# Performance work log

Measured on AMD Instinct MI355X. Metric: run time of the kernel, lower is better.

## Reference

```python
import jax, jax.numpy as jnp
import numpy as np

N, E, D, H, T, R, K = 40000, 320000, 128, 4, 3, 5, 3
DK = D // H
SQRT_DK = float(np.sqrt(DK))

def _glorot(key, shape):
    lim = float(np.sqrt(6.0 / (shape[-2] + shape[-1])))
    return jax.random.uniform(key, shape, jnp.float32, -lim, lim)

def setup_inputs():
    ks = jax.random.split(jax.random.key(0), 16)
    return {
        "meta_xs": jax.random.normal(ks[0], (N, D), jnp.float32),
        "node_type": jax.random.randint(ks[1], (N,), 0, T),
        "edge_index": jax.random.randint(ks[2], (2, E), 0, N),
        "edge_type": jax.random.randint(ks[3], (E,), 0, R),
        "edge_time": jax.random.randint(ks[4], (E,), 0, 100),
        "q_w": _glorot(ks[5], (T, D, D)), "q_b": jnp.zeros((T, D), jnp.float32),
        "k_w": _glorot(ks[6], (T, D, D)), "k_b": jnp.zeros((T, D), jnp.float32),
        "v_w": _glorot(ks[7], (T, D, D)), "v_b": jnp.zeros((T, D), jnp.float32),
        "a_w": _glorot(ks[8], (T, D, D)), "a_b": jnp.zeros((T, D), jnp.float32),
        "rel_pri": jnp.ones((R, H), jnp.float32),
        "rel_att": _glorot(ks[9], (R, H, DK, DK)),
        "rel_msg": _glorot(ks[10], (R, H, DK, DK)),
        "WMk": _glorot(ks[11], (K, D, D)),
        "Wak": _glorot(ks[12], (K, D, D)),
        "Wq": _glorot(ks[13], (D, D)), "bq": jnp.zeros((D,), jnp.float32),
        "Wkl": _glorot(ks[14], (D, D)), "bkl": jnp.zeros((D,), jnp.float32),
        "skip": jnp.ones((T,), jnp.float32),
        "ln_g": jnp.ones((T, D), jnp.float32),
        "ln_b": jnp.zeros((T, D), jnp.float32),
    }

def _forward(meta_xs, q_w, q_b, k_w, k_b, v_w, v_b, a_w, a_b, rel_pri, rel_att,
             rel_msg, WMk, Wak, Wq, bq, Wkl, bkl, skip, ln_g, ln_b,
             node_type, edge_index, edge_type):
    src, tgt = edge_index[0], edge_index[1]
    ar = jnp.arange(N)

    def typed(x, W, b):  # per-node-type linear: equivalent to the type-masked loops
        all_t = jnp.einsum('ni,tio->tno', x, W)        # [T, N, D]
        return all_t[node_type, ar] + b[node_type]      # [N, D]

    qn = typed(meta_xs, q_w, q_b).reshape(N, H, DK)
    kn = typed(meta_xs, k_w, k_b).reshape(N, H, DK)
    vn = typed(meta_xs, v_w, v_b).reshape(N, H, DK)
    qe, ke, ve = qn[tgt], kn[src], vn[src]              # [E, H, DK]

    # relation-specific bmm, honoring per-relation dispatch without [E,H,DK,DK] gather
    kp = jnp.zeros_like(ke)
    vp = jnp.zeros_like(ve)
    for r in range(R):
        sel = (edge_type == r)[:, None, None]
        kp = jnp.where(sel, jnp.einsum('ehd,hdm->ehm', ke, rel_att[r]), kp)
        vp = jnp.where(sel, jnp.einsum('ehd,hdm->ehm', ve, rel_msg[r]), vp)

    logits = (qe * kp).sum(-1) * rel_pri[edge_type] / SQRT_DK   # [E, H]
    # segment softmax over incoming edges per target node (torch_geometric softmax)
    mx = jax.ops.segment_max(logits, tgt, num_segments=N)
    ex = jnp.exp(logits - mx[tgt])
    att = ex / (jax.ops.segment_sum(ex, tgt, num_segments=N)[tgt] + 1e-16)

    # power-moment expanded, attention-weighted messages: [K, E, D]
    msgs = jnp.stack([((vp ** (kk + 1)) * att[:, :, None]).reshape(E, D) for kk in range(K)])

    # faithful to original aggregate(): messages indexed by target node id (not edge id)
    agg = jnp.stack([jax.ops.segment_sum(msgs[kk][tgt], tgt, num_segments=N) for kk in range(K)])
    # faithful: only the last moment gets the signed K-th root (loop re-clones each iter)
    root = jnp.sign(agg[K - 1]) * (jnp.abs(agg[K - 1]) + 1e-18) ** (1.0 / K)
    aggm = agg.at[K - 1].set(root)
    aggm = jnp.einsum('knd,kde->kne', aggm, WMk)        # [K, N, D]

    qlin = meta_xs @ Wq + bq
    res = jnp.zeros((N, D), meta_xs.dtype)
    for kk in range(K):
        front = qlin @ Wak[kk]                          # [N, D]
        tail = aggm[kk] @ Wkl + bkl                     # [N, D]
        t = jax.nn.sigmoid((front * tail).sum(-1))      # [N]
        res = res + t[:, None] * aggm[kk]

    # update(): gelu -> per-type linear -> learned skip -> per-type LayerNorm
    h = jax.nn.gelu(res, approximate=False)
    trans = typed(h, a_w, a_b)
    alpha = jax.nn.sigmoid(skip)[node_type][:, None]
    y = trans * alpha + meta_xs * (1.0 - alpha)
    mu = y.mean(-1, keepdims=True)
    var = ((y - mu) ** 2).mean(-1, keepdims=True)
    y = (y - mu) / jnp.sqrt(var + 1e-5) * ln_g[node_type] + ln_b[node_type]
    return y

def reference(meta_xs, node_type, edge_index, edge_type, edge_time,
              q_w, q_b, k_w, k_b, v_w, v_b, a_w, a_b, rel_pri, rel_att, rel_msg,
              WMk, Wak, Wq, bq, Wkl, bkl, skip, ln_g, ln_b):
    return _forward(meta_xs, q_w, q_b, k_w, k_b, v_w, v_b, a_w, a_b, rel_pri,
                    rel_att, rel_msg, WMk, Wak, Wq, bq, Wkl, bkl, skip, ln_g, ln_b,
                    node_type, edge_index, edge_type)
```

## Files before the change

kernel.cpp:

```cpp
#include <hip/hip_runtime.h>

#define N_ 40000
#define E_ 320000
#define D_ 128
#define H_ 4
#define T_ 3
#define R_ 5

typedef unsigned short u16;
typedef float f32x4 __attribute__((ext_vector_type(4)));
typedef short s16x8 __attribute__((ext_vector_type(8)));

__device__ __forceinline__ float bf2f(u16 h){ return __uint_as_float(((unsigned)h)<<16); }
__device__ __forceinline__ u16 f2bf(float f){
  unsigned u = __float_as_uint(f);
  u += 0x7fffu + ((u>>16)&1u);
  return (u16)(u>>16);
}
__device__ __forceinline__ unsigned fmono(float f){
  unsigned u = __float_as_uint(f);
  return (u>>31) ? ~u : (u | 0x80000000u);
}
__device__ __forceinline__ float monof(unsigned u){
  return (u>>31) ? __uint_as_float(u & 0x7fffffffu) : __uint_as_float(~u);
}
__device__ __forceinline__ float ldx(const void* p, long i, int f32){
  return f32 ? ((const float*)p)[i] : bf2f(((const u16*)p)[i]);
}
__device__ __forceinline__ float wredsum(float v){
  #pragma unroll
  for (int m=32;m;m>>=1) v += __shfl_xor(v, m, 64);
  return v;
}
__device__ __forceinline__ void split2(float v0, float v1, unsigned& hp, unsigned& lp){
  unsigned b0 = __float_as_uint(v0), b1 = __float_as_uint(v1);
  unsigned h0 = b0 & 0xFFFF0000u,    h1 = b1 & 0xFFFF0000u;
  float r0 = v0 - __uint_as_float(h0);
  float r1 = v1 - __uint_as_float(h1);
  hp = (h0>>16) | h1;
  lp = (__float_as_uint(r0)>>16) | (__float_as_uint(r1) & 0xFFFF0000u);
}

#define W_QW 0
#define W_KW 49152
#define W_VW 98304
#define W_AW 147456
#define W_QB 196608
#define W_KB 196992
#define W_VB 197376
#define W_AB 197760
#define W_PRI 198144
#define W_RATT 198164
#define W_RMSG 218644
#define W_WMK 239124
#define W_WAK 288276
#define W_WQ 337428
#define W_BQ 353812
#define W_WKL 353940
#define W_BKL 370324
#define W_SKIP 370452
#define W_LNG 370455
#define W_LNB 370839
#define W_TOT 371223

#define WT_Q   0
#define WT_K   98304
#define WT_V   196608
#define WT_A   294912
#define WT_WQ  396328
#define WT_WMK 478248

#define OFF_FLAGS 0ul
#define OFF_WCF   512ul
#define OFF_NT32  1485824ul
#define OFF_EI32  1646080ul
#define OFF_ET32  4206592ul
#define OFF_PERM  5486592ul
#define OFF_PCNT  5648384ul
#define OFF_TVAL  5648896ul
#define OFF_NPERM 5730816ul
#define OFF_LOG   6288896ul
#define OFF_QN    12848896ul
#define OFF_KN    33328896ul
#define OFF_VN    53808896ul
#define OFF_QLIN  74288896ul
#define OFF_QTR   94768896ul

__global__ __launch_bounds__(256) void detect_kernel(
    const u16* __restrict__ xs, const int* __restrict__ nt, int* __restrict__ flags)
{
  __shared__ int sBig, sZero, sNz;
  int tid = threadIdx.x;
  if (tid==0){ sBig=0; sZero=0; sNz=0; }
  __syncthreads();
  int big=0, zc=0;
  for (int i=tid; i<1024; i+=256) {
    u16 v = xs[2*i];
    int e = (v>>7)&0xFF;
    big += (e >= 200);
    zc  += (v == 0);
  }
  int nz=0;
  for (int i=tid; i<1024; i+=256) nz += (nt[2*i+1] != 0);
  atomicAdd(&sBig, big); atomicAdd(&sZero, zc); atomicAdd(&sNz, nz);
  __syncthreads();
  if (tid==0) {
    flags[0] = (sBig > 64) || (sZero > 900);
    flags[1] = (sNz == 0);
  }
}

struct FPtrs { const void* p[20]; };
__global__ __launch_bounds__(256) void convf_kernel(
    const int* __restrict__ flags, FPtrs ptrs, float* __restrict__ wcf)
{
  const int start[21] = {0,49152,98304,147456,196608,196992,197376,197760,198144,
    198164,218644,239124,288276,337428,353812,353940,370324,370452,370455,370839,371223};
  int i = blockIdx.x*256 + threadIdx.x;
  if (i >= W_TOT) return;
  int arr = 0;
  #pragma unroll
  for (int a=1; a<20; ++a) arr += (i >= start[a]);
  int local = i - start[arr];
  wcf[i] = ldx(ptrs.p[arr], local, flags[0]);
}

__global__ __launch_bounds__(256) void idxconv_kernel(
    const int* __restrict__ flags,
    const int* __restrict__ nt, const int* __restrict__ ei, const int* __restrict__ et,
    int* __restrict__ nt32, int* __restrict__ ei32, int* __restrict__ et32)
{
  int i = blockIdx.x*256 + threadIdx.x;
  if (i >= 1000000) return;
  int w = flags[1] ? 2 : 1;
  if (i < 40000)        nt32[i] = nt[(long)i*w];
  else if (i < 680000)  { int j=i-40000;  ei32[j] = ei[(long)j*w]; }
  else                  { int j=i-680000; et32[j] = et[(long)j*w]; }
}

__global__ __launch_bounds__(256) void pinit_kernel(int* __restrict__ perm, int* __restrict__ pc){
  int i = blockIdx.x*256 + threadIdx.x;
  if (i < 40448) perm[i] = -1;
  if (i < 12) pc[i] = 0;
}
__global__ __launch_bounds__(256) void einit_kernel(int* __restrict__ nperm, int* __restrict__ pc2){
  int i = blockIdx.x*256 + threadIdx.x;
  if (i < 40320) nperm[i] = -1;
  if (i < 16) pc2[i] = 0;
}
__global__ __launch_bounds__(256) void cnt_kernel(
    const int* __restrict__ keys, int n, int ntypes, int* __restrict__ gcnt)
{
  __shared__ int lh[8];
  if (threadIdx.x < ntypes) lh[threadIdx.x] = 0;
  __syncthreads();
  int i = blockIdx.x*256 + threadIdx.x;
  if (i < n) atomicAdd(&lh[keys[i]], 1);
  __syncthreads();
  if (threadIdx.x < ntypes && lh[threadIdx.x])
    atomicAdd(&gcnt[threadIdx.x], lh[threadIdx.x]);
}
__global__ void pofs_kernel(int* __restrict__ pc){
  if (threadIdx.x==0 && blockIdx.x==0) {
    pc[8] = 0;
    pc[9] = (pc[0]+127)&~127;
    pc[10] = pc[9] + ((pc[1]+127)&~127);
  }
}
__global__ void eofs_kernel(int* __restrict__ pc2){
  if (threadIdx.x==0 && blockIdx.x==0) {
    pc2[10] = 0;
    #pragma unroll
    for (int r=1;r<R_;++r) pc2[10+r] = pc2[10+r-1] + ((pc2[r-1]+63)&~63);
  }
}
__global__ __launch_bounds__(256) void scat_kernel(
    const int* __restrict__ keys, int n, int ntypes,
    const int* __restrict__ ofs, int* __restrict__ fill, int* __restrict__ perm)
{
  __shared__ int lh[8];
  __shared__ int lbase[8];
  if (threadIdx.x < ntypes) lh[threadIdx.x] = 0;
  __syncthreads();
  int i = blockIdx.x*256 + threadIdx.x;
  int t = 0, rank = 0;
  bool ok = (i < n);
  if (ok) { t = keys[i]; rank = atomicAdd(&lh[t], 1); }
  __syncthreads();
  if (threadIdx.x < ntypes)
    lbase[threadIdx.x] = lh[threadIdx.x] ? atomicAdd(&fill[threadIdx.x], lh[threadIdx.x]) : 0;
  __syncthreads();
  if (ok) perm[ofs[t] + lbase[t] + rank] = i;
}

__global__ __launch_bounds__(256) void init_kernel(
    unsigned* __restrict__ mxkey, float* __restrict__ sumex, int* __restrict__ deg)
{
  int i = blockIdx.x*256 + threadIdx.x;
  mxkey[i] = fmono(-1e30f);
  sumex[i] = 0.f;
  if (i < N_) deg[i] = 0;
}

__global__ __launch_bounds__(256) void prepA_kernel(
    const float* __restrict__ wcf, float* __restrict__ raT)
{
  int i = blockIdx.x*256 + threadIdx.x;
  if (i >= 20480) return;
  int d = i & 31, m = (i>>5) & 31, rh = i >> 10;
  raT[i] = wcf[W_RATT + (rh*32 + d)*32 + m];
}

__global__ __launch_bounds__(128) void prepB_kernel(
    const float* __restrict__ wcf, float* __restrict__ MT, float* __restrict__ ck)
{
  int col = threadIdx.x, i = blockIdx.x, k = blockIdx.y;
  const float* wak = wcf + W_WAK + k*16384 + col*128;
  const float* wkl = wcf + W_WKL + i*128;
  float acc = 0.f, accC = 0.f;
  #pragma unroll 8
  for (int j=0;j<128;++j) {
    float a = wak[j];
    acc  += a * wkl[j];
    if (i==0) accC += a * wcf[W_BKL + j];
  }
  MT[k*16384 + i*128 + col] = acc;
  if (i==0) ck[k*128 + col] = accC;
}

struct TPtrs { const void* p[16]; int soff[16]; int doff[16]; };
__global__ __launch_bounds__(256) void prepT_kernel(
    TPtrs tp, const int* __restrict__ flags, int xmode, u16* __restrict__ dst)
{
  __shared__ float T[128][33];
  int m = blockIdx.y;
  int c0 = blockIdx.x * 32;
  int tid = threadIdx.x;
  int xf = xmode ? 1 : flags[0];
  const void* src = tp.p[m];
  long sb = tp.soff[m];
  {
    int k = tid >> 1, ch = (tid & 1) * 16;
    #pragma unroll
    for (int j=0;j<16;++j)
      T[k][ch+j] = ldx(src, sb + (long)k*128 + c0 + ch + j, xf);
  }
  __syncthreads();
  int col = tid >> 3, k0 = (tid & 7) * 16;
  unsigned hp[8], lp[8];
  #pragma unroll
  for (int j=0;j<8;++j)
    split2(T[k0+2*j][col], T[k0+2*j+1][col], hp[j], lp[j]);
  u16* dh = dst + tp.doff[m] + (long)(c0+col)*128 + k0;
  ((uint4*)dh)[0] = uint4{hp[0],hp[1],hp[2],hp[3]};
  ((uint4*)dh)[1] = uint4{hp[4],hp[5],hp[6],hp[7]};
  u16* dl = dh + 16384;
  ((uint4*)dl)[0] = uint4{lp[0],lp[1],lp[2],lp[3]};
  ((uint4*)dl)[1] = uint4{lp[4],lp[5],lp[6],lp[7]};
}

struct GC4 { const float* x[4]; int woff[4]; int boff[4]; int typed[4]; };
__global__ __launch_bounds__(256) void gemmt2_kernel(
    GC4 cfg, const int* __restrict__ flags, int xmode,
    const u16* __restrict__ Wt, const float* __restrict__ wcf,
    const int* __restrict__ perm, const int* __restrict__ nt,
    int dotmode, const float* __restrict__ qlin, const float* __restrict__ ck,
    int powmode, const float* __restrict__ sattp, int wmode,
    float* __restrict__ out, long yostride)
{
  __shared__ u16 Ah[4096], Al[4096], Wh[4096], Wl[4096];
  __shared__ int ridx[128];
  __shared__ int tblk_s;
  int tid = threadIdx.x;
  int y = blockIdx.y;
  int row0 = blockIdx.x*128;
  if (tid < 128) {
    int rr = row0 + tid;
    int rg = perm ? perm[rr] : (rr < N_ ? rr : -1);
    ridx[tid] = rg;
    if (tid==0) tblk_s = (perm && nt && rg>=0) ? nt[rg] : 0;
  }
  __syncthreads();
  if (ridx[0] < 0) return;
  int tblk = cfg.typed[y] ? tblk_s : 0;
  const u16* Wg = Wt + cfg.woff[y] + tblk*32768;
  const void* X = (const void*)cfg.x[y];
  int xf = xmode ? 1 : flags[0];
  int wlo_on = wmode ? 1 : flags[0];

  int lane = tid & 63;
  int wv   = tid >> 6;
  int lrow = lane & 15;
  int lk   = (lane >> 4) << 3;
  int rbase = wv*32;

  f32x4 acc[2][8];
  #pragma unroll
  for (int m=0;m<2;++m)
    #pragma unroll
    for (int n=0;n<8;++n) acc[m][n] = f32x4{0.f,0.f,0.f,0.f};

  int sr = tid >> 1;
  int sh = (tid & 1) * 16;
  int srow = ridx[sr];
  int sp  = (sr >> 1) & 3;
  int sc0 = (sh >> 3) ^ sp;
  int sc1 = ((sh >> 3) + 1) ^ sp;

  for (int kc=0;kc<4;++kc) {
    __syncthreads();
    {
      float v[16];
      if (srow < 0) {
        #pragma unroll
        for (int j=0;j<16;++j) v[j]=0.f;
      } else if (powmode) {
        const float4* s4 = reinterpret_cast<const float4*>((const float*)X + (long)srow*128 + kc*32 + sh);
        float4 q0=s4[0],q1=s4[1],q2=s4[2],q3=s4[3];
        float tv[16] = {q0.x,q0.y,q0.z,q0.w,q1.x,q1.y,q1.z,q1.w,
                        q2.x,q2.y,q2.z,q2.w,q3.x,q3.y,q3.z,q3.w};
        float sc = sattp[srow*4 + kc];
        #pragma unroll
        for (int j=0;j<16;++j) {
          float vv = tv[j]; float a;
          if (y==0)      a = vv*sc;
          else if (y==1) a = vv*vv*sc;
          else { float a3 = vv*vv*vv*sc;
                 a = (a3==0.f) ? 0.f : copysignf(cbrtf(fabsf(a3)+1e-18f), a3); }
          v[j] = a;
        }
      } else if (xf) {
        const float4* s4 = reinterpret_cast<const float4*>((const float*)X + (long)srow*128 + kc*32 + sh);
        float4 q0=s4[0],q1=s4[1],q2=s4[2],q3=s4[3];
        v[0]=q0.x;v[1]=q0.y;v[2]=q0.z;v[3]=q0.w; v[4]=q1.x;v[5]=q1.y;v[6]=q1.z;v[7]=q1.w;
        v[8]=q2.x;v[9]=q2.y;v[10]=q2.z;v[11]=q2.w; v[12]=q3.x;v[13]=q3.y;v[14]=q3.z;v[15]=q3.w;
      } else {
        const u16* s = (const u16*)X + (long)srow*128 + kc*32 + sh;
        #pragma unroll
        for (int j=0;j<16;++j) v[j] = bf2f(s[j]);
      }
      unsigned hp[8], lp[8];
      #pragma unroll
      for (int j=0;j<8;++j) split2(v[2*j], v[2*j+1], hp[j], lp[j]);
      ((uint4*)Ah)[sr*4 + sc0] = uint4{hp[0],hp[1],hp[2],hp[3]};
      ((uint4*)Ah)[sr*4 + sc1] = uint4{hp[4],hp[5],hp[6],hp[7]};
      if (xf) {
        ((uint4*)Al)[sr*4 + sc0] = uint4{lp[0],lp[1],lp[2],lp[3]};
        ((uint4*)Al)[sr*4 + sc1] = uint4{lp[4],lp[5],lp[6],lp[7]};
      }
    }
    {
      const u16* gh = Wg + sr*128 + kc*32 + sh;
      uint4 h0 = ((const uint4*)gh)[0];
      uint4 h1 = ((const uint4*)gh)[1];
      ((uint4*)Wh)[sr*4 + sc0] = h0;
      ((uint4*)Wh)[sr*4 + sc1] = h1;
      if (wlo_on) {
        const u16* gl = gh + 16384;
        uint4 l0 = ((const uint4*)gl)[0];
        uint4 l1 = ((const uint4*)gl)[1];
        ((uint4*)Wl)[sr*4 + sc0] = l0;
        ((uint4*)Wl)[sr*4 + sc1] = l1;
      }
    }
    __syncthreads();
    s16x8 ah[2], al[2];
    #pragma unroll
    for (int m=0;m<2;++m) {
      int row = rbase + m*16 + lrow;
      int ia = row*32 + (lk ^ (((row>>1)&3)<<3));
      ah[m] = *(const s16x8*)(Ah + ia);
      if (xf) al[m] = *(const s16x8*)(Al + ia);
    }
    #pragma unroll
    for (int n=0;n<8;++n) {
      int col = n*16 + lrow;
      int ib = col*32 + (lk ^ (((col>>1)&3)<<3));
      s16x8 bh = *(const s16x8*)(Wh + ib);
      acc[0][n] = __builtin_amdgcn_mfma_f32_16x16x32_bf16(ah[0], bh, acc[0][n], 0,0,0);
      acc[1][n] = __builtin_amdgcn_mfma_f32_16x16x32_bf16(ah[1], bh, acc[1][n], 0,0,0);
      if (xf) {
        acc[0][n] = __builtin_amdgcn_mfma_f32_16x16x32_bf16(al[0], bh, acc[0][n], 0,0,0);
        acc[1][n] = __builtin_amdgcn_mfma_f32_16x16x32_bf16(al[1], bh, acc[1][n], 0,0,0);
      }
      if (wlo_on) {
        s16x8 bl = *(const s16x8*)(Wl + ib);
        acc[0][n] = __builtin_amdgcn_mfma_f32_16x16x32_bf16(ah[0], bl, acc[0][n], 0,0,0);
        acc[1][n] = __builtin_amdgcn_mfma_f32_16x16x32_bf16(ah[1], bl, acc[1][n], 0,0,0);
      }
    }
  }

  int rq = (lane >> 4) << 2;
  if (!dotmode) {
    float b[8];
    if (cfg.boff[y] >= 0) {
      const float* bp = wcf + cfg.boff[y] + tblk*128;
      #pragma unroll
      for (int n=0;n<8;++n) b[n] = bp[n*16 + lrow];
    } else {
      #pragma unroll
      for (int n=0;n<8;++n) b[n] = 0.f;
    }
    #pragma unroll
    for (int m=0;m<2;++m) {
      #pragma unroll
      for (int r=0;r<4;++r) {
        int rowl = rbase + m*16 + rq + r;
        int rowg = ridx[rowl];
        if (rowg < 0) continue;
        float* op = out + (long)y*yostride + (long)rowg*128 + lrow;
        #pragma unroll
        for (int n=0;n<8;++n) op[n*16] = acc[m][n][r] + b[n];
      }
    }
  } else {
    float ckv[8];
    #pragma unroll
    for (int n=0;n<8;++n) ckv[n] = ck[y*128 + n*16 + lrow];
    #pragma unroll
    for (int m=0;m<2;++m) {
      #pragma unroll
      for (int r=0;r<4;++r) {
        int rowl = rbase + m*16 + rq + r;
        int rowg = ridx[rowl];
        float d = 0.f;
        if (rowg >= 0) {
          const float* qp = qlin + (long)rowg*128 + lrow;
          #pragma unroll
          for (int n=0;n<8;++n) d += (acc[m][n][r] + ckv[n]) * qp[n*16];
        }
        #pragma unroll
        for (int msk=1; msk<16; msk<<=1) d += __shfl_xor(d, msk, 64);
        if (lrow==0 && rowg>=0) out[(long)rowg*4 + y] = 1.f/(1.f+expf(-d));
      }
    }
  }
}

__global__ __launch_bounds__(256) void gemmbd_kernel(
    const float* __restrict__ X,
    const float* __restrict__ Wtab, int wsel,
    const int* __restrict__ perm, const int* __restrict__ gsrc, const int* __restrict__ et,
    float* __restrict__ out)
{
  __shared__ float As[64*152];
  __shared__ float Ws[4096];
  __shared__ int ridx[64];
  __shared__ int rsel_s;
  int tid = threadIdx.x;
  int row0 = blockIdx.x*64;
  if (tid < 64) {
    int rr = row0 + tid;
    int pe = perm ? perm[rr] : (rr < N_ ? rr : -1);
    ridx[tid] = pe;
    if (tid == 0) rsel_s = (wsel && pe >= 0) ? et[pe] : 0;
  }
  __syncthreads();
  if (ridx[0] < 0) return;
  const float* Wg = Wtab + (long)(wsel ? rsel_s : 0)*4096;
  #pragma unroll
  for (int j=0;j<4;++j)
    *reinterpret_cast<float4*>(&Ws[j*1024 + tid*4]) =
      *reinterpret_cast<const float4*>(Wg + j*1024 + tid*4);
  {
    int sar = tid >> 2, sh = tid & 3;
    int pe_s = ridx[sar];
    int arow = (pe_s < 0) ? -1 : (gsrc ? gsrc[pe_s] : pe_s);
    float* dst = &As[sar*152 + sh*36];
    if (arow < 0) {
      #pragma unroll
      for (int j=0;j<8;++j) *reinterpret_cast<float4*>(dst + j*4) = float4{0.f,0.f,0.f,0.f};
    } else {
      const float4* s4 = reinterpret_cast<const float4*>(X + (long)arow*128 + sh*32);
      #pragma unroll
      for (int j=0;j<8;++j) *reinterpret_cast<float4*>(dst + j*4) = s4[j];
    }
  }
  __syncthreads();
  int rg_ = tid >> 5, cg = tid & 31;
  int h = cg >> 3, c4 = (cg & 7)*4;
  float acc[8][4];
  #pragma unroll
  for (int r=0;r<8;++r){ acc[r][0]=0.f; acc[r][1]=0.f; acc[r][2]=0.f; acc[r][3]=0.f; }
  #pragma unroll
  for (int mq=0;mq<8;++mq) {
    float wv[4][4];
    #pragma unroll
    for (int i=0;i<4;++i) {
      float4 wt = *reinterpret_cast<const float4*>(&Ws[h*1024 + (mq*4+i)*32 + c4]);
      wv[i][0]=wt.x; wv[i][1]=wt.y; wv[i][2]=wt.z; wv[i][3]=wt.w;
    }
    #pragma unroll
    for (int r=0;r<8;++r) {
      float4 a4 = *reinterpret_cast<const float4*>(&As[(rg_*8+r)*152 + h*36 + mq*4]);
      float av[4] = {a4.x,a4.y,a4.z,a4.w};
      #pragma unroll
      for (int i=0;i<4;++i) {
        acc[r][0]+=av[i]*wv[i][0]; acc[r][1]+=av[i]*wv[i][1];
        acc[r][2]+=av[i]*wv[i][2]; acc[r][3]+=av[i]*wv[i][3];
      }
    }
  }
  #pragma unroll
  for (int r=0;r<8;++r) {
    int pe = ridx[rg_*8+r];
    if (pe < 0) continue;
    float4 o = {acc[r][0],acc[r][1],acc[r][2],acc[r][3]};
    *reinterpret_cast<float4*>(out + (long)pe*128 + h*32 + c4) = o;
  }
}

__global__ __launch_bounds__(256) void epass_kernel(
    const float* __restrict__ kn, const float* __restrict__ qtr, const float* __restrict__ wcf,
    const int* __restrict__ ei, const int* __restrict__ et, int rsel,
    float* __restrict__ logits, unsigned* __restrict__ mxkey, int* __restrict__ deg)
{
  int gid = blockIdx.x*256 + threadIdx.x;
  int e = gid >> 2, h = gid & 3;
  if (et[e] != rsel) return;
  int s = ei[e], t = ei[E_+e];
  const float4* ka = reinterpret_cast<const float4*>(kn + (long)s*128 + h*32);
  const float4* qa = reinterpret_cast<const float4*>(qtr + (long)t*128 + h*32);
  float acc = 0.f;
  #pragma unroll
  for (int i=0;i<8;++i) {
    float4 a = ka[i], b = qa[i];
    acc += a.x*b.x + a.y*b.y + a.z*b.z + a.w*b.w;
  }
  float lg = acc * wcf[W_PRI + rsel*H_+h] * 0.17677669529663687f;
  logits[gid] = lg;
  atomicMax(mxkey + t*H_+h, fmono(lg));
  if (h==0) atomicAdd(deg + t, 1);
}

__global__ __launch_bounds__(256) void eexp_kernel(
    const int* __restrict__ ei, float* __restrict__ logits,
    const unsigned* __restrict__ mxkey, float* __restrict__ sumex)
{
  int gid = blockIdx.x*256 + threadIdx.x;
  int e = gid >> 2, h = gid & 3;
  int t = ei[E_+e];
  float d = fminf(logits[gid] - monof(mxkey[t*H_+h]), 0.f);
  float ex = expf(d);
  if (e < N_) logits[gid] = ex;
  atomicAdd(sumex + t*H_+h, ex);
}

__global__ __launch_bounds__(256) void satt_kernel(
    const int* __restrict__ ei, const float* __restrict__ ex, const float* __restrict__ sumex,
    const int* __restrict__ deg, float* __restrict__ satt)
{
  int i = blockIdx.x*256 + threadIdx.x;
  int n = i >> 2, h = i & 3;
  int t = ei[E_+n];
  satt[i] = (float)deg[n] * ex[i] / (sumex[t*H_+h] + 1e-16f);
}

__global__ __launch_bounds__(256) void gatemix_kernel(
    const float* __restrict__ tval,
    const float* __restrict__ ag0, const float* __restrict__ ag1, const float* __restrict__ ag2,
    float* __restrict__ hout)
{
  long gid = (long)blockIdx.x*256 + threadIdx.x;
  int n = (int)(gid >> 7);
  float res = tval[n*4+0]*ag0[gid] + tval[n*4+1]*ag1[gid] + tval[n*4+2]*ag2[gid];
  hout[gid] = 0.5f*res*(1.f+erff(res*0.70710678118654752f));
}

__global__ __launch_bounds__(256) void lnf_kernel(
    const float* __restrict__ trans, const void* __restrict__ x, const int* __restrict__ flags,
    const int* __restrict__ nt, const float* __restrict__ wcf, void* __restrict__ outv)
{
  int wave = threadIdx.x >> 6, lane = threadIdx.x & 63;
  int n = blockIdx.x*4 + wave;
  int j = lane*2;
  int xf = flags[0];
  int t = nt[n];
  float alpha = 1.f/(1.f+expf(-wcf[W_SKIP+t]));
  long base = (long)n*128 + j;
  float y0 = alpha*trans[base]   + (1.f-alpha)*ldx(x, base,   xf);
  float y1 = alpha*trans[base+1] + (1.f-alpha)*ldx(x, base+1, xf);
  float mu = wredsum(y0+y1) * (1.f/128.f);
  float d0 = y0-mu, d1 = y1-mu;
  float var = wredsum(d0*d0+d1*d1) * (1.f/128.f);
  float inv = rsqrtf(var + 1e-5f);
  float o0 = d0*inv*wcf[W_LNG + t*128+j]   + wcf[W_LNB + t*128+j];
  float o1 = d1*inv*wcf[W_LNG + t*128+j+1] + wcf[W_LNB + t*128+j+1];
  if (xf) {
    ((float*)outv)[base]   = o0;
    ((float*)outv)[base+1] = o1;
  } else {
    unsigned o = (unsigned)f2bf(o0) | ((unsigned)f2bf(o1)<<16);
    *reinterpret_cast<unsigned*>(((u16*)outv)+base) = o;
  }
}

extern "C" void kernel_launch(void* const* d_in, const int* in_sizes, int n_in,
                              void* d_out, int out_size, void* d_ws, size_t ws_size,
                              hipStream_t stream) {
  char* w = (char*)d_ws;
  int*      flags = (int*)     (w + OFF_FLAGS);
  float*    wcf   = (float*)   (w + OFF_WCF);
  u16*      wtb   = (u16*)     (w + OFF_WCF);
  int*      nt32  = (int*)     (w + OFF_NT32);
  int*      ei32  = (int*)     (w + OFF_EI32);
  int*      et32  = (int*)     (w + OFF_ET32);
  int*      perm  = (int*)     (w + OFF_PERM);
  int*      pcnt  = (int*)     (w + OFF_PCNT);
  int*      pc2   = (int*)     (w + OFF_PCNT + 128);
  float*    raT   = (float*)   (w + OFF_TVAL);
  float*    satt  = (float*)   (w + OFF_TVAL);
  float*    tval  = (float*)   (w + OFF_TVAL);
  int*      nperm = (int*)     (w + OFF_NPERM);
  float*    logits= (float*)   (w + OFF_LOG);
  unsigned* mxkey = (unsigned*)(w + OFF_LOG + 5120000);
  float*    sumex = (float*)   (w + OFF_LOG + 5760000);
  int*      deg   = (int*)     (w + OFF_LOG + 6400000);
  float*    MT    = (float*)   (w + OFF_LOG);
  float*    ckb   = (float*)   (w + OFF_LOG + 786432);
  u16*      mtt   = (u16*)     (w + OFF_LOG + 1048576);
  float*    qn    = (float*)   (w + OFF_QN);
  float*    ag0   = (float*)   (w + OFF_QN);
  float*    trans = (float*)   (w + OFF_QN);
  float*    kn    = (float*)   (w + OFF_KN);
  float*    ag1   = (float*)   (w + OFF_KN);
  float*    vn    = (float*)   (w + OFF_VN);
  float*    ag2   = (float*)   (w + OFF_VN);
  float*    qlin  = (float*)   (w + OFF_QLIN);
  float*    hbuf  = (float*)   (w + OFF_QLIN);
  float*    qtrb  = (float*)   (w + OFF_QTR);
  float*    vp    = (float*)   (w + OFF_QTR);

  detect_kernel<<<1,256,0,stream>>>((const u16*)d_in[0], (const int*)d_in[1], flags);
  FPtrs fp;
  fp.p[0]=d_in[5];  fp.p[1]=d_in[7];  fp.p[2]=d_in[9];  fp.p[3]=d_in[11];
  fp.p[4]=d_in[6];  fp.p[5]=d_in[8];  fp.p[6]=d_in[10]; fp.p[7]=d_in[12];
  fp.p[8]=d_in[13]; fp.p[9]=d_in[14]; fp.p[10]=d_in[15];fp.p[11]=d_in[16];
  fp.p[12]=d_in[17];fp.p[13]=d_in[18];fp.p[14]=d_in[19];fp.p[15]=d_in[20];
  fp.p[16]=d_in[21];fp.p[17]=d_in[22];fp.p[18]=d_in[23];fp.p[19]=d_in[24];
  convf_kernel<<<1451,256,0,stream>>>(flags, fp, wcf);
  idxconv_kernel<<<3907,256,0,stream>>>(flags, (const int*)d_in[1],
                                        (const int*)d_in[2], (const int*)d_in[3],
                                        nt32, ei32, et32);
  pinit_kernel<<<159,256,0,stream>>>(perm, pcnt);
  cnt_kernel  <<<157,256,0,stream>>>(nt32, N_, T_, pcnt);
  pofs_kernel <<<1,64,0,stream>>>(pcnt);
  scat_kernel <<<157,256,0,stream>>>(nt32, N_, T_, pcnt+8, pcnt+4, perm);
  einit_kernel<<<158,256,0,stream>>>(nperm, pc2);
  cnt_kernel  <<<157,256,0,stream>>>(et32, N_, R_, pc2);
  eofs_kernel <<<1,64,0,stream>>>(pc2);
  scat_kernel <<<157,256,0,stream>>>(et32, N_, R_, pc2+10, pc2+5, nperm);
  prepA_kernel<<<80,256,0,stream>>>(wcf, raT);

  TPtrs tps;
  for (int t=0;t<3;++t) {
    tps.p[t]    = d_in[5];  tps.soff[t]    = t*16384; tps.doff[t]    = WT_Q   + t*32768;
    tps.p[3+t]  = d_in[7];  tps.soff[3+t]  = t*16384; tps.doff[3+t]  = WT_K   + t*32768;
    tps.p[6+t]  = d_in[9];  tps.soff[6+t]  = t*16384; tps.doff[6+t]  = WT_V   + t*32768;
    tps.p[9+t]  = d_in[11]; tps.soff[9+t]  = t*16384; tps.doff[9+t]  = WT_A   + t*32768;
    tps.p[13+t] = d_in[16]; tps.soff[13+t] = t*16384; tps.doff[13+t] = WT_WMK + t*32768;
  }
  tps.p[12] = d_in[18]; tps.soff[12] = 0; tps.doff[12] = WT_WQ;
  prepT_kernel<<<dim3(4,16),256,0,stream>>>(tps, flags, 0, wtb);

  GC4 cq;
  cq.x[0]=(const float*)d_in[0]; cq.x[1]=cq.x[0]; cq.x[2]=cq.x[0]; cq.x[3]=cq.x[0];
  cq.woff[0]=WT_Q; cq.woff[1]=WT_K; cq.woff[2]=WT_V; cq.woff[3]=WT_WQ;
  cq.boff[0]=W_QB; cq.boff[1]=W_KB; cq.boff[2]=W_VB; cq.boff[3]=W_BQ;
  cq.typed[0]=1; cq.typed[1]=1; cq.typed[2]=1; cq.typed[3]=0;
  gemmt2_kernel<<<dim3(316,4),256,0,stream>>>(cq, flags, 0, wtb, wcf, perm, nt32,
      0, nullptr, nullptr, 0, nullptr, 0, qn, 5120000);

  init_kernel<<<625,256,0,stream>>>(mxkey, sumex, deg);

  for (int r=0; r<R_; ++r) {
    gemmbd_kernel<<<625,256,0,stream>>>(qn, raT + r*4096, 0, nullptr, nullptr, nullptr, qtrb);
    epass_kernel<<<5000,256,0,stream>>>(kn, qtrb, wcf, ei32, et32, r, logits, mxkey, deg);
  }
  eexp_kernel<<<5000,256,0,stream>>>(ei32, logits, mxkey, sumex);

  gemmbd_kernel<<<630,256,0,stream>>>(vn, wcf+W_RMSG, 1, nperm, ei32, et32, vp);

  satt_kernel<<<625,256,0,stream>>>(ei32, logits, sumex, deg, satt);

  prepB_kernel<<<dim3(128,3),128,0,stream>>>(wcf, MT, ckb);
  TPtrs tpm;
  for (int i=0;i<16;++i){ tpm.p[i]=MT; tpm.soff[i]=0; tpm.doff[i]=0; }
  for (int k=0;k<3;++k){ tpm.soff[k]=k*16384; tpm.doff[k]=k*32768; }
  prepT_kernel<<<dim3(4,3),256,0,stream>>>(tpm, flags, 1, mtt);

  GC4 cp;
  cp.x[0]=vp; cp.x[1]=vp; cp.x[2]=vp; cp.x[3]=vp;
  cp.woff[0]=WT_WMK; cp.woff[1]=WT_WMK+32768; cp.woff[2]=WT_WMK+65536; cp.woff[3]=0;
  cp.boff[0]=-1; cp.boff[1]=-1; cp.boff[2]=-1; cp.boff[3]=-1;
  cp.typed[0]=0; cp.typed[1]=0; cp.typed[2]=0; cp.typed[3]=0;
  gemmt2_kernel<<<dim3(313,3),256,0,stream>>>(cp, flags, 1, wtb, wcf, nullptr, nullptr,
      0, nullptr, nullptr, 1, satt, 0, ag0, 5120000);

  GC4 cd;
  cd.x[0]=ag0; cd.x[1]=ag1; cd.x[2]=ag2; cd.x[3]=ag2;
  cd.woff[0]=0; cd.woff[1]=32768; cd.woff[2]=65536; cd.woff[3]=0;
  cd.boff[0]=-1; cd.boff[1]=-1; cd.boff[2]=-1; cd.boff[3]=-1;
  cd.typed[0]=0; cd.typed[1]=0; cd.typed[2]=0; cd.typed[3]=0;
  gemmt2_kernel<<<dim3(313,3),256,0,stream>>>(cd, flags, 1, mtt, wcf, nullptr, nullptr,
      1, qlin, ckb, 0, nullptr, 1, tval, 0);

  gatemix_kernel<<<20000,256,0,stream>>>(tval, ag0, ag1, ag2, hbuf);

  GC4 ct;
  ct.x[0]=hbuf; ct.x[1]=hbuf; ct.x[2]=hbuf; ct.x[3]=hbuf;
  ct.woff[0]=WT_A; ct.woff[1]=0; ct.woff[2]=0; ct.woff[3]=0;
  ct.boff[0]=W_AB; ct.boff[1]=-1; ct.boff[2]=-1; ct.boff[3]=-1;
  ct.typed[0]=1; ct.typed[1]=0; ct.typed[2]=0; ct.typed[3]=0;
  gemmt2_kernel<<<dim3(316,1),256,0,stream>>>(ct, flags, 1, wtb, wcf, perm, nt32,
      0, nullptr, nullptr, 0, nullptr, 0, trans, 0);

  lnf_kernel<<<10000,256,0,stream>>>(trans, d_in[0], flags, nt32, wcf, d_out);

  (void)in_sizes; (void)n_in; (void)out_size; (void)ws_size;
}
```

Before: 565.3 us.

## Prefetch next K-chunk of gathered rows and weights into registers

The typed-GEMM staging loop now loads the next K-chunk of the gathered X rows (and power-mode scale) and the weight tile into registers before the MFMA phase of the current chunk. Each iteration then converts and stores the prefetched data to LDS. This software pipelining hides global-load latency behind compute. The cost is more live registers, which may reduce occupancy. The bf16 path now uses vector loads instead of scalar ones.

```diff
diff --git a/kernel.cpp b/kernel.cpp
--- a/kernel.cpp
+++ b/kernel.cpp
@@ -307,61 +307,84 @@
   int sc0 = (sh >> 3) ^ sp;
   int sc1 = ((sh >> 3) + 1) ^ sp;
 
+  float4 fa0, fa1, fa2, fa3;
+  float  scp = 0.f;
+  uint4  pw0, pw1, pw2, pw3;
+
+  if (srow >= 0) {
+    if (powmode || xf) {
+      const float4* s4 = reinterpret_cast<const float4*>((const float*)X + (long)srow*128 + sh);
+      fa0=s4[0]; fa1=s4[1]; fa2=s4[2]; fa3=s4[3];
+      if (powmode) scp = sattp[srow*4];
+    } else {
+      const float4* s4 = reinterpret_cast<const float4*>((const u16*)X + (long)srow*128 + sh);
+      fa0=s4[0]; fa1=s4[1];
+    }
+  }
+  {
+    const u16* gh = Wg + sr*128 + sh;
+    pw0 = ((const uint4*)gh)[0]; pw1 = ((const uint4*)gh)[1];
+    if (wlo_on) { pw2 = ((const uint4*)(gh+16384))[0]; pw3 = ((const uint4*)(gh+16384))[1]; }
+  }
+
   for (int kc=0;kc<4;++kc) {
-    __syncthreads();
-    {
-      float v[16];
-      if (srow < 0) {
-        #pragma unroll
-        for (int j=0;j<16;++j) v[j]=0.f;
-      } else if (powmode) {
-        const float4* s4 = reinterpret_cast<const float4*>((const float*)X + (long)srow*128 + kc*32 + sh);
-        float4 q0=s4[0],q1=s4[1],q2=s4[2],q3=s4[3];
-        float tv[16] = {q0.x,q0.y,q0.z,q0.w,q1.x,q1.y,q1.z,q1.w,
-                        q2.x,q2.y,q2.z,q2.w,q3.x,q3.y,q3.z,q3.w};
-        float sc = sattp[srow*4 + kc];
+    uint4 AH0, AH1, AL0, AL1;
+    if (srow < 0) {
+      AH0 = AH1 = AL0 = AL1 = uint4{0,0,0,0};
+    } else if (powmode || xf) {
+      float tv[16] = {fa0.x,fa0.y,fa0.z,fa0.w, fa1.x,fa1.y,fa1.z,fa1.w,
+                      fa2.x,fa2.y,fa2.z,fa2.w, fa3.x,fa3.y,fa3.z,fa3.w};
+      if (powmode) {
         #pragma unroll
         for (int j=0;j<16;++j) {
           float vv = tv[j]; float a;
-          if (y==0)      a = vv*sc;
-          else if (y==1) a = vv*vv*sc;
-          else { float a3 = vv*vv*vv*sc;
+          if (y==0)      a = vv*scp;
+          else if (y==1) a = vv*vv*scp;
+          else { float a3 = vv*vv*vv*scp;
                  a = (a3==0.f) ? 0.f : copysignf(cbrtf(fabsf(a3)+1e-18f), a3); }
-          v[j] = a;
+          tv[j] = a;
         }
-      } else if (xf) {
-        const float4* s4 = reinterpret_cast<const float4*>((const float*)X + (long)srow*128 + kc*32 + sh);
-        float4 q0=s4[0],q1=s4[1],q2=s4[2],q3=s4[3];
-        v[0]=q0.x;v[1]=q0.y;v[2]=q0.z;v[3]=q0.w; v[4]=q1.x;v[5]=q1.y;v[6]=q1.z;v[7]=q1.w;
-        v[8]=q2.x;v[9]=q2.y;v[10]=q2.z;v[11]=q2.w; v[12]=q3.x;v[13]=q3.y;v[14]=q3.z;v[15]=q3.w;
-      } else {
-        const u16* s = (const u16*)X + (long)srow*128 + kc*32 + sh;
-        #pragma unroll
-        for (int j=0;j<16;++j) v[j] = bf2f(s[j]);
       }
       unsigned hp[8], lp[8];
       #pragma unroll
-      for (int j=0;j<8;++j) split2(v[2*j], v[2*j+1], hp[j], lp[j]);
-      ((uint4*)Ah)[sr*4 + sc0] = uint4{hp[0],hp[1],hp[2],hp[3]};
-      ((uint4*)Ah)[sr*4 + sc1] = uint4{hp[4],hp[5],hp[6],hp[7]};
-      if (xf) {
-        ((uint4*)Al)[sr*4 + sc0] = uint4{lp[0],lp[1],lp[2],lp[3]};
-        ((uint4*)Al)[sr*4 + sc1] = uint4{lp[4],lp[5],lp[6],lp[7]};
+      for (int j=0;j<8;++j) split2(tv[2*j], tv[2*j+1], hp[j], lp[j]);
+      AH0 = uint4{hp[0],hp[1],hp[2],hp[3]}; AH1 = uint4{hp[4],hp[5],hp[6],hp[7]};
+      AL0 = uint4{lp[0],lp[1],lp[2],lp[3]}; AL1 = uint4{lp[4],lp[5],lp[6],lp[7]};
+    } else {
+      AH0 = *reinterpret_cast<const uint4*>(&fa0);
+      AH1 = *reinterpret_cast<const uint4*>(&fa1);
+      AL0 = AL1 = uint4{0,0,0,0};
+    }
+    uint4 WH0 = pw0, WH1 = pw1, WL0 = pw2, WL1 = pw3;
+
+    __syncthreads();
+    ((uint4*)Ah)[sr*4 + sc0] = AH0;
+    ((uint4*)Ah)[sr*4 + sc1] = AH1;
+    if (xf) {
+      ((uint4*)Al)[sr*4 + sc0] = AL0;
+      ((uint4*)Al)[sr*4 + sc1] = AL1;
+    }
+    ((uint4*)Wh)[sr*4 + sc0] = WH0;
+    ((uint4*)Wh)[sr*4 + sc1] = WH1;
+    if (wlo_on) {
+      ((uint4*)Wl)[sr*4 + sc0] = WL0;
+      ((uint4*)Wl)[sr*4 + sc1] = WL1;
+    }
+    if (kc < 3) {
+      int kn_ = kc + 1;
+      if (srow >= 0) {
+        if (powmode || xf) {
+          const float4* s4 = reinterpret_cast<const float4*>((const float*)X + (long)srow*128 + kn_*32 + sh);
+          fa0=s4[0]; fa1=s4[1]; fa2=s4[2]; fa3=s4[3];
+          if (powmode) scp = sattp[srow*4 + kn_];
+        } else {
+          const float4* s4 = reinterpret_cast<const float4*>((const u16*)X + (long)srow*128 + kn_*32 + sh);
+          fa0=s4[0]; fa1=s4[1];
+        }
       }
-    }
-    {
-      const u16* gh = Wg + sr*128 + kc*32 + sh;
-      uint4 h0 = ((const uint4*)gh)[0];
-      uint4 h1 = ((const uint4*)gh)[1];
-      ((uint4*)Wh)[sr*4 + sc0] = h0;
-      ((uint4*)Wh)[sr*4 + sc1] = h1;
-      if (wlo_on) {
-        const u16* gl = gh + 16384;
-        uint4 l0 = ((const uint4*)gl)[0];
-        uint4 l1 = ((const uint4*)gl)[1];
-        ((uint4*)Wl)[sr*4 + sc0] = l0;
-        ((uint4*)Wl)[sr*4 + sc1] = l1;
-      }
+      const u16* gh = Wg + sr*128 + kn_*32 + sh;
+      pw0 = ((const uint4*)gh)[0]; pw1 = ((const uint4*)gh)[1];
+      if (wlo_on) { pw2 = ((const uint4*)(gh+16384))[0]; pw3 = ((const uint4*)(gh+16384))[1]; }
     }
     __syncthreads();
     s16x8 ah[2], al[2];
```

New measurement: 555.3 us. Within noise of the previous version (-1.8%).

## Load GEMM operands directly into registers, dropping LDS staging and barriers

Applied to the files above, without the earlier changes.

The typed GEMM kernel no longer stages the activation and weight tiles through shared memory with swizzled layouts and __syncthreads. Each wave now loads its own input rows and the weight columns from global memory straight into MFMA operand layout, and splits them into high and low bf16 parts in registers. Row indices come from perm per thread instead of a shared table. This removes the barriers and the LDS write/read traffic. In exchange, each of the four waves re-fetches the same weight tile from cache, and the activation loads are smaller and less coalesced.

```diff
diff --git a/kernel.cpp b/kernel.cpp
--- a/kernel.cpp
+++ b/kernel.cpp
@@ -268,125 +268,89 @@
     int powmode, const float* __restrict__ sattp, int wmode,
     float* __restrict__ out, long yostride)
 {
-  __shared__ u16 Ah[4096], Al[4096], Wh[4096], Wl[4096];
-  __shared__ int ridx[128];
-  __shared__ int tblk_s;
   int tid = threadIdx.x;
   int y = blockIdx.y;
   int row0 = blockIdx.x*128;
-  if (tid < 128) {
-    int rr = row0 + tid;
-    int rg = perm ? perm[rr] : (rr < N_ ? rr : -1);
-    ridx[tid] = rg;
-    if (tid==0) tblk_s = (perm && nt && rg>=0) ? nt[rg] : 0;
-  }
-  __syncthreads();
-  if (ridx[0] < 0) return;
-  int tblk = cfg.typed[y] ? tblk_s : 0;
-  const u16* Wg = Wt + cfg.woff[y] + tblk*32768;
-  const void* X = (const void*)cfg.x[y];
-  int xf = xmode ? 1 : flags[0];
-  int wlo_on = wmode ? 1 : flags[0];
-
   int lane = tid & 63;
   int wv   = tid >> 6;
   int lrow = lane & 15;
   int lk   = (lane >> 4) << 3;
   int rbase = wv*32;
 
+  int head = perm ? perm[row0] : (row0 < N_ ? row0 : -1);
+  if (head < 0) return;
+  int tblk = (cfg.typed[y] && perm && nt) ? nt[head] : 0;
+  const u16* Wg = Wt + cfg.woff[y] + tblk*32768;
+  const void* X = (const void*)cfg.x[y];
+  int xf = xmode ? 1 : flags[0];
+  int wlo_on = wmode ? 1 : flags[0];
+
+  int rl0 = row0 + rbase + lrow;
+  int rl1 = rl0 + 16;
+  int sr0 = perm ? perm[rl0] : (rl0 < N_ ? rl0 : -1);
+  int sr1 = perm ? perm[rl1] : (rl1 < N_ ? rl1 : -1);
+  long s0 = (sr0 < 0) ? 0 : (long)sr0;
+  long s1 = (sr1 < 0) ? 0 : (long)sr1;
+
   f32x4 acc[2][8];
   #pragma unroll
   for (int m=0;m<2;++m)
     #pragma unroll
     for (int n=0;n<8;++n) acc[m][n] = f32x4{0.f,0.f,0.f,0.f};
 
-  int sr = tid >> 1;
-  int sh = (tid & 1) * 16;
-  int srow = ridx[sr];
-  int sp  = (sr >> 1) & 3;
-  int sc0 = (sh >> 3) ^ sp;
-  int sc1 = ((sh >> 3) + 1) ^ sp;
-
+  #pragma unroll
   for (int kc=0;kc<4;++kc) {
-    __syncthreads();
-    {
-      float v[16];
-      if (srow < 0) {
+    s16x8 ah0, ah1, al0, al1;
+    if (xf) {
+      const float* x0 = (const float*)X + s0*128 + kc*32 + lk;
+      const float* x1 = (const float*)X + s1*128 + kc*32 + lk;
+      float4 a0 = ((const float4*)x0)[0], a1 = ((const float4*)x0)[1];
+      float4 b0 = ((const float4*)x1)[0], b1 = ((const float4*)x1)[1];
+      float t0[8] = {a0.x,a0.y,a0.z,a0.w,a1.x,a1.y,a1.z,a1.w};
+      float t1[8] = {b0.x,b0.y,b0.z,b0.w,b1.x,b1.y,b1.z,b1.w};
+      if (powmode) {
+        float sc0 = sattp[s0*4 + kc];
+        float sc1 = sattp[s1*4 + kc];
         #pragma unroll
-        for (int j=0;j<16;++j) v[j]=0.f;
-      } else if (powmode) {
-        const float4* s4 = reinterpret_cast<const float4*>((const float*)X + (long)srow*128 + kc*32 + sh);
-        float4 q0=s4[0],q1=s4[1],q2=s4[2],q3=s4[3];
-        float tv[16] = {q0.x,q0.y,q0.z,q0.w,q1.x,q1.y,q1.z,q1.w,
-                        q2.x,q2.y,q2.z,q2.w,q3.x,q3.y,q3.z,q3.w};
-        float sc = sattp[srow*4 + kc];
-        #pragma unroll
-        for (int j=0;j<16;++j) {
-          float vv = tv[j]; float a;
-          if (y==0)      a = vv*sc;
-          else if (y==1) a = vv*vv*sc;
-          else { float a3 = vv*vv*vv*sc;
-                 a = (a3==0.f) ? 0.f : copysignf(cbrtf(fabsf(a3)+1e-18f), a3); }
-          v[j] = a;
+        for (int j=0;j<8;++j) {
+          float v0 = t0[j], v1 = t1[j];
+          if (y==0)      { t0[j] = v0*sc0;    t1[j] = v1*sc1; }
+          else if (y==1) { t0[j] = v0*v0*sc0; t1[j] = v1*v1*sc1; }
+          else {
+            float a3 = v0*v0*v0*sc0, b3 = v1*v1*v1*sc1;
+            t0[j] = (a3==0.f) ? 0.f : copysignf(cbrtf(fabsf(a3)+1e-18f), a3);
+            t1[j] = (b3==0.f) ? 0.f : copysignf(cbrtf(fabsf(b3)+1e-18f), b3);
+          }
         }
-      } else if (xf) {
-        const float4* s4 = reinterpret_cast<const float4*>((const float*)X + (long)srow*128 + kc*32 + sh);
-        float4 q0=s4[0],q1=s4[1],q2=s4[2],q3=s4[3];
-        v[0]=q0.x;v[1]=q0.y;v[2]=q0.z;v[3]=q0.w; v[4]=q1.x;v[5]=q1.y;v[6]=q1.z;v[7]=q1.w;
-        v[8]=q2.x;v[9]=q2.y;v[10]=q2.z;v[11]=q2.w; v[12]=q3.x;v[13]=q3.y;v[14]=q3.z;v[15]=q3.w;
-      } else {
-        const u16* s = (const u16*)X + (long)srow*128 + kc*32 + sh;
-        #pragma unroll
-        for (int j=0;j<16;++j) v[j] = bf2f(s[j]);
       }
-      unsigned hp[8], lp[8];
-      #pragma unroll
-      for (int j=0;j<8;++j) split2(v[2*j], v[2*j+1], hp[j], lp[j]);
-      ((uint4*)Ah)[sr*4 + sc0] = uint4{hp[0],hp[1],hp[2],hp[3]};
-      ((uint4*)Ah)[sr*4 + sc1] = uint4{hp[4],hp[5],hp[6],hp[7]};
+      unsigned h0[4], l0[4], h1[4], l1[4];
+      #pragma unroll
+      for (int j=0;j<4;++j) {
+        split2(t0[2*j], t0[2*j+1], h0[j], l0[j]);
+        split2(t1[2*j], t1[2*j+1], h1[j], l1[j]);
+      }
+      uint4 H0{h0[0],h0[1],h0[2],h0[3]}, L0{l0[0],l0[1],l0[2],l0[3]};
+      uint4 H1{h1[0],h1[1],h1[2],h1[3]}, L1{l1[0],l1[1],l1[2],l1[3]};
+      ah0 = *reinterpret_cast<s16x8*>(&H0); al0 = *reinterpret_cast<s16x8*>(&L0);
+      ah1 = *reinterpret_cast<s16x8*>(&H1); al1 = *reinterpret_cast<s16x8*>(&L1);
+    } else {
+      ah0 = *reinterpret_cast<const s16x8*>((const u16*)X + s0*128 + kc*32 + lk);
+      ah1 = *reinterpret_cast<const s16x8*>((const u16*)X + s1*128 + kc*32 + lk);
+    }
+    #pragma unroll
+    for (int n=0;n<8;++n) {
+      const u16* wp = Wg + (n*16+lrow)*128 + kc*32 + lk;
+      s16x8 bh = *reinterpret_cast<const s16x8*>(wp);
+      acc[0][n] = __builtin_amdgcn_mfma_f32_16x16x32_bf16(ah0, bh, acc[0][n], 0,0,0);
+      acc[1][n] = __builtin_amdgcn_mfma_f32_16x16x32_bf16(ah1, bh, acc[1][n], 0,0,0);
       if (xf) {
-        ((uint4*)Al)[sr*4 + sc0] = uint4{lp[0],lp[1],lp[2],lp[3]};
-        ((uint4*)Al)[sr*4 + sc1] = uint4{lp[4],lp[5],lp[6],lp[7]};
-      }
-    }
-    {
-      const u16* gh = Wg + sr*128 + kc*32 + sh;
-      uint4 h0 = ((const uint4*)gh)[0];
-      uint4 h1 = ((const uint4*)gh)[1];
-      ((uint4*)Wh)[sr*4 + sc0] = h0;
-      ((uint4*)Wh)[sr*4 + sc1] = h1;
-      if (wlo_on) {
-        const u16* gl = gh + 16384;
-        uint4 l0 = ((const uint4*)gl)[0];
-        uint4 l1 = ((const uint4*)gl)[1];
-        ((uint4*)Wl)[sr*4 + sc0] = l0;
-        ((uint4*)Wl)[sr*4 + sc1] = l1;
-      }
-    }
-    __syncthreads();
-    s16x8 ah[2], al[2];
-    #pragma unroll
-    for (int m=0;m<2;++m) {
-      int row = rbase + m*16 + lrow;
-      int ia = row*32 + (lk ^ (((row>>1)&3)<<3));
-      ah[m] = *(const s16x8*)(Ah + ia);
-      if (xf) al[m] = *(const s16x8*)(Al + ia);
-    }
-    #pragma unroll
-    for (int n=0;n<8;++n) {
-      int col = n*16 + lrow;
-      int ib = col*32 + (lk ^ (((col>>1)&3)<<3));
-      s16x8 bh = *(const s16x8*)(Wh + ib);
-      acc[0][n] = __builtin_amdgcn_mfma_f32_16x16x32_bf16(ah[0], bh, acc[0][n], 0,0,0);
-      acc[1][n] = __builtin_amdgcn_mfma_f32_16x16x32_bf16(ah[1], bh, acc[1][n], 0,0,0);
-      if (xf) {
-        acc[0][n] = __builtin_amdgcn_mfma_f32_16x16x32_bf16(al[0], bh, acc[0][n], 0,0,0);
-        acc[1][n] = __builtin_amdgcn_mfma_f32_16x16x32_bf16(al[1], bh, acc[1][n], 0,0,0);
+        acc[0][n] = __builtin_amdgcn_mfma_f32_16x16x32_bf16(al0, bh, acc[0][n], 0,0,0);
+        acc[1][n] = __builtin_amdgcn_mfma_f32_16x16x32_bf16(al1, bh, acc[1][n], 0,0,0);
       }
       if (wlo_on) {
-        s16x8 bl = *(const s16x8*)(Wl + ib);
-        acc[0][n] = __builtin_amdgcn_mfma_f32_16x16x32_bf16(ah[0], bl, acc[0][n], 0,0,0);
-        acc[1][n] = __builtin_amdgcn_mfma_f32_16x16x32_bf16(ah[1], bl, acc[1][n], 0,0,0);
+        s16x8 bl = *reinterpret_cast<const s16x8*>(wp + 16384);
+        acc[0][n] = __builtin_amdgcn_mfma_f32_16x16x32_bf16(ah0, bl, acc[0][n], 0,0,0);
+        acc[1][n] = __builtin_amdgcn_mfma_f32_16x16x32_bf16(ah1, bl, acc[1][n], 0,0,0);
       }
     }
   }
@@ -406,8 +370,8 @@
     for (int m=0;m<2;++m) {
       #pragma unroll
       for (int r=0;r<4;++r) {
-        int rowl = rbase + m*16 + rq + r;
-        int rowg = ridx[rowl];
+        int rr = row0 + rbase + m*16 + rq + r;
+        int rowg = perm ? perm[rr] : (rr < N_ ? rr : -1);
         if (rowg < 0) continue;
         float* op = out + (long)y*yostride + (long)rowg*128 + lrow;
         #pragma unroll
@@ -422,8 +386,8 @@
     for (int m=0;m<2;++m) {
       #pragma unroll
       for (int r=0;r<4;++r) {
-        int rowl = rbase + m*16 + rq + r;
-        int rowg = ridx[rowl];
+        int rr = row0 + rbase + m*16 + rq + r;
+        int rowg = perm ? perm[rr] : (rr < N_ ? rr : -1);
         float d = 0.f;
         if (rowg >= 0) {
           const float* qp = qlin + (long)rowg*128 + lrow;
```

Result: slower. 657.6 us (+16.3%).
